# Kernel optimization log

Measured on AMD Instinct MI355X. Metric: run time of the kernel, lower is better.

The kernel has to match this reference:

```python
import jax, jax.numpy as jnp
import numpy as np

B, T, C = 4, 2048, 2048
N_HEAD, N_KV = 16, 4
HEAD_DIM = C // N_HEAD          # 128
KV_DIM = HEAD_DIM * N_KV        # 512
WINDOW = 256
ROPE_BASE = 10000.0


def setup_inputs() -> dict:
    key = jax.random.key(0)
    ks = jax.random.split(key, 5)
    s = 0.02
    return {
        "x": jax.random.normal(ks[0], (B, T, C), dtype=jnp.float32),
        "Wq": jax.random.normal(ks[1], (C, C), dtype=jnp.float32) * s,
        "Wk": jax.random.normal(ks[2], (C, KV_DIM), dtype=jnp.float32) * s,
        "Wv": jax.random.normal(ks[3], (C, KV_DIM), dtype=jnp.float32) * s,
        "Wo": jax.random.normal(ks[4], (C, C), dtype=jnp.float32) * s,
    }


def _rope(x):
    # x: [B, H, T, D]; GPT-NeoX half-split rotation
    d = x.shape[-1]
    t = x.shape[-2]
    inv_freq = 1.0 / (ROPE_BASE ** (jnp.arange(0, d, 2, dtype=jnp.float32) / d))
    freqs = jnp.arange(t, dtype=jnp.float32)[:, None] * inv_freq[None, :]  # [T, D/2]
    cos, sin = jnp.cos(freqs), jnp.sin(freqs)
    x1, x2 = x[..., : d // 2], x[..., d // 2:]
    return jnp.concatenate([x1 * cos - x2 * sin, x1 * sin + x2 * cos], axis=-1)


def reference(x, Wq, Wk, Wv, Wo):
    b, t, c = x.shape
    hd = HEAD_DIM
    q = (x @ Wq).reshape(b, t, N_HEAD, hd).transpose(0, 2, 1, 3)   # [B,nh,T,hd]
    k = (x @ Wk).reshape(b, t, N_KV, hd).transpose(0, 2, 1, 3)     # [B,nkv,T,hd]
    v = (x @ Wv).reshape(b, t, N_KV, hd).transpose(0, 2, 1, 3)

    q = _rope(q)
    k = _rope(k)

    # GQA: repeat kv heads to match query heads
    rep = N_HEAD // N_KV
    k = jnp.repeat(k, rep, axis=1)   # [B,nh,T,hd]
    v = jnp.repeat(v, rep, axis=1)

    att = jnp.einsum("bhqd,bhkd->bhqk", q, k) / jnp.sqrt(jnp.float32(hd))
    i = jnp.arange(t)[:, None]
    j = jnp.arange(t)[None, :]
    # causal AND sliding window: i - WINDOW <= j <= i
    mask = (j <= i) & (j >= i - WINDOW)
    att = jnp.where(mask[None, None], att, jnp.finfo(att.dtype).min)
    att = jax.nn.softmax(att, axis=-1)

    y = jnp.einsum("bhqk,bhkd->bhqd", att, v)          # [B,nh,T,hd]
    y = y.transpose(0, 2, 1, 3).reshape(b, t, c)       # [B,T,C]
    return y @ Wo
```

## Files before the change

### kernel.cpp

```cpp
#include <hip/hip_runtime.h>
#include <stdint.h>

#define T_ 2048
#define C_ 2048
#define HD 128
#define LDQKV 3072

typedef unsigned short u16;
typedef __attribute__((ext_vector_type(8))) short bf16x8;
typedef __attribute__((ext_vector_type(4))) float f32x4;
typedef __attribute__((ext_vector_type(4))) float float4v;
typedef __attribute__((ext_vector_type(4))) u16 u16x4;
typedef __attribute__((ext_vector_type(8))) u16 u16x8;

typedef __attribute__((address_space(3))) void lds_void;
typedef const __attribute__((address_space(1))) void gbl_void;

__device__ __forceinline__ void gload_lds16(const void* g, void* l) {
  __builtin_amdgcn_global_load_lds((gbl_void*)(uintptr_t)g,
                                   (lds_void*)(uint32_t)(uintptr_t)l, 16, 0, 0);
}

__device__ __forceinline__ u16 f2bf(float f) {
  union { float f; uint32_t u; } v; v.f = f;
  uint32_t r = v.u + 0x7FFFu + ((v.u >> 16) & 1u);
  return (u16)(r >> 16);
}
__device__ __forceinline__ float bf2f(u16 h) {
  union { uint32_t u; float f; } v; v.u = ((uint32_t)h) << 16;
  return v.f;
}

#define BAR() do { asm volatile("" ::: "memory"); __builtin_amdgcn_s_barrier(); asm volatile("" ::: "memory"); } while (0)
#define VMCNT(n) asm volatile("s_waitcnt vmcnt(" #n ")" ::: "memory")
#define LGKM0()  asm volatile("s_waitcnt lgkmcnt(0)" ::: "memory")

__global__ __launch_bounds__(256) void k_conv_x(const float* __restrict__ x, u16* __restrict__ o) {
  size_t idx = (size_t)blockIdx.x * 256 + threadIdx.x;
  float4v xv = *(const float4v*)(x + idx * 4);
  u16x4 r;
#pragma unroll
  for (int e = 0; e < 4; ++e) r[e] = f2bf(xv[e]);
  *(u16x4*)(o + idx * 4) = r;
}

__device__ __forceinline__ void ttile(const float* __restrict__ src, int ldw, int nb,
                                      int k0, int n0out, u16* __restrict__ out, int tid,
                                      float (*Lt)[68]) {
  int kr = tid >> 4, nc = (tid & 15) * 4;
#pragma unroll
  for (int s = 0; s < 4; ++s) {
    float4v v = *(const float4v*)(src + (size_t)(k0 + kr + 16 * s) * ldw + nb + nc);
#pragma unroll
    for (int e = 0; e < 4; ++e) Lt[kr + 16 * s][nc + e] = v[e];
  }
  __syncthreads();
  int nr = tid & 31, kc = (tid >> 5) * 8;
#pragma unroll
  for (int s2 = 0; s2 < 2; ++s2) {
    int n = nr + 32 * s2;
    u16x8 o;
#pragma unroll
    for (int e = 0; e < 8; ++e) o[e] = f2bf(Lt[kc + e][n]);
    *(u16x8*)(out + (size_t)(n0out + n) * 2048 + k0 + kc) = o;
  }
}

__global__ __launch_bounds__(256) void k_wt_qkv(const float* __restrict__ Wq, const float* __restrict__ Wk,
                                                const float* __restrict__ Wv, u16* __restrict__ wt) {
  __shared__ float Lt[64][68];
  const int n0 = blockIdx.x * 64, k0 = blockIdx.y * 64;
  const float* src; int ldw, nb;
  if (n0 < 2048)      { src = Wq; ldw = 2048; nb = n0; }
  else if (n0 < 2560) { src = Wk; ldw = 512;  nb = n0 - 2048; }
  else                { src = Wv; ldw = 512;  nb = n0 - 2560; }
  ttile(src, ldw, nb, k0, n0, wt, threadIdx.x, Lt);
}

__global__ __launch_bounds__(256) void k_wo_t(const float* __restrict__ Wo, u16* __restrict__ wt) {
  __shared__ float Lt[64][68];
  ttile(Wo, 2048, blockIdx.x * 64, blockIdx.y * 64, blockIdx.x * 64, wt, threadIdx.x, Lt);
}

__global__ __launch_bounds__(256) void k_cs(float* __restrict__ cst) {
  int idx = blockIdx.x * 256 + threadIdx.x;
  int t = idx >> 6, d = idx & 63;
  float inv = expf(-(float)d * (1.0f / 64.0f) * 9.2103403719761836f);
  float f = (float)t * inv;
  float s, c;
  sincosf(f, &s, &c);
  cst[idx * 2] = c;
  cst[idx * 2 + 1] = s;
}

__global__ __launch_bounds__(256) void k_rope(u16* __restrict__ qkv, const float* __restrict__ cst) {
  int idx = blockIdx.x * 256 + threadIdx.x;
  int token = idx / 160;
  int rem = idx - token * 160;
  int hd = rem >> 3, oct = rem & 7;
  int col = ((hd < 16) ? hd * 128 : 2048 + (hd - 16) * 128) + oct * 8;
  size_t base = (size_t)token * LDQKV + col;
  int t = token & (T_ - 1);
  float sc = (hd < 16) ? 0.08838834764831845f : 1.0f;
  u16x8 a = *(const u16x8*)(qkv + base);
  u16x8 b2 = *(const u16x8*)(qkv + base + 64);
  const float* cp = cst + (size_t)(t * 64 + oct * 8) * 2;
  u16x8 ra, rb;
#pragma unroll
  for (int e = 0; e < 8; ++e) {
    float c = cp[e * 2], s = cp[e * 2 + 1];
    float x1 = bf2f(a[e]), x2 = bf2f(b2[e]);
    ra[e] = f2bf((x1 * c - x2 * s) * sc);
    rb[e] = f2bf((x1 * s + x2 * c) * sc);
  }
  *(u16x8*)(qkv + base) = ra;
  *(u16x8*)(qkv + base + 64) = rb;
}

#define READ_A(mf, ks) (*(const bf16x8*)&As_[(wm * 128 + (mf) * 16 + l15) * 64 + ((((ks) * 4 + lhi) ^ (l15 & 7)) * 8)])
#define READ_B(nf, ks) (*(const bf16x8*)&Bs_[(wn * 64 + (nf) * 16 + l15) * 64 + ((((ks) * 4 + lhi) ^ (l15 & 7)) * 8)])
#define MFMA_QUAD(Q)                                                          \
  _Pragma("unroll") for (int mi = 0; mi < 2; ++mi)                            \
  _Pragma("unroll") for (int nf = 0; nf < 4; ++nf)                            \
  _Pragma("unroll") for (int ks = 0; ks < 2; ++ks)                            \
      acc[(Q) * 2 + mi][nf] = __builtin_amdgcn_mfma_f32_16x16x32_bf16(        \
          af[(Q) * 2 + mi][ks], bb[nf][ks], acc[(Q) * 2 + mi][nf], 0, 0, 0);

template<int OUTF32>
__global__ __launch_bounds__(512, 2) void k_gemm8(const u16* __restrict__ A, const u16* __restrict__ Bt,
                                                  void* __restrict__ Cout, int M, int N, int K, int nbx) {
  __shared__ __attribute__((aligned(16))) u16 lds[2][2][256 * 64];
  const int tid = threadIdx.x, lane = tid & 63;
  const int w = tid >> 6, wm = w >> 2, wn = w & 3;
  const int l15 = lane & 15, lhi = lane >> 4;
  const int nwg = gridDim.x, cpx = nwg >> 3;
  const int wg = (blockIdx.x & 7) * cpx + (blockIdx.x >> 3);
  const int bx = wg % nbx, by = wg / nbx;
  const int m0 = by * 256, n0 = bx * 256;
  const int NT = K >> 6;

  auto STAGE = [&](int half, int tt) {
    const u16* src = (half < 2) ? A : Bt;
    const int r0 = ((half < 2) ? m0 : n0) + (half & 1) * 128;
    u16* dst = &lds[tt & 1][half >> 1][(half & 1) * 8192];
    const int kk = tt * 64;
#pragma unroll
    for (int it = 0; it < 2; ++it) {
      int c = it * 512 + tid;
      int row = c >> 3, kc = c & 7;
      gload_lds16(src + (size_t)(r0 + row) * K + kk + ((kc ^ (row & 7)) * 8), dst + c * 8);
    }
  };

  f32x4 acc[8][4];
#pragma unroll
  for (int i = 0; i < 8; ++i)
#pragma unroll
    for (int j = 0; j < 4; ++j) acc[i][j] = (f32x4){0.f, 0.f, 0.f, 0.f};

  STAGE(0, 0); STAGE(1, 0); STAGE(2, 0); STAGE(3, 0);
  STAGE(0, 1); STAGE(1, 1); STAGE(2, 1);
  VMCNT(6);
  BAR();

  for (int t = 0; t < NT; ++t) {
    const u16* As_ = lds[t & 1][0];
    const u16* Bs_ = lds[t & 1][1];
    bf16x8 af[8][2], bb[4][2];
#pragma unroll
    for (int nf = 0; nf < 4; ++nf) { bb[nf][0] = READ_B(nf, 0); bb[nf][1] = READ_B(nf, 1); }
#pragma unroll
    for (int mf = 0; mf < 2; ++mf) { af[mf][0] = READ_A(mf, 0); af[mf][1] = READ_A(mf, 1); }
    if (t + 1 < NT) STAGE(3, t + 1);
    BAR();
    __builtin_amdgcn_s_setprio(1);
    MFMA_QUAD(0);
    __builtin_amdgcn_s_setprio(0);
    BAR();
#pragma unroll
    for (int mf = 2; mf < 8; ++mf) { af[mf][0] = READ_A(mf, 0); af[mf][1] = READ_A(mf, 1); }
    if (t + 2 < NT) STAGE(2, t + 2);
    BAR();
    __builtin_amdgcn_s_setprio(1);
    MFMA_QUAD(1);
    __builtin_amdgcn_s_setprio(0);
    LGKM0();
    BAR();
    if (t + 2 < NT) STAGE(0, t + 2);
    BAR();
    __builtin_amdgcn_s_setprio(1);
    MFMA_QUAD(2);
    __builtin_amdgcn_s_setprio(0);
    BAR();
    if (t + 2 < NT) STAGE(1, t + 2);
    BAR();
    __builtin_amdgcn_s_setprio(1);
    MFMA_QUAD(3);
    __builtin_amdgcn_s_setprio(0);
    if (t + 2 < NT) { VMCNT(6); } else { VMCNT(0); }
    BAR();
  }

#pragma unroll
  for (int mf = 0; mf < 8; ++mf) {
#pragma unroll
    for (int nf = 0; nf < 4; ++nf) {
      int col = n0 + wn * 64 + nf * 16 + l15;
#pragma unroll
      for (int r = 0; r < 4; ++r) {
        int row = m0 + wm * 128 + mf * 16 + lhi * 4 + r;
        float v = acc[mf][nf][r];
        if (OUTF32) ((float*)Cout)[(size_t)row * N + col] = v;
        else        ((u16*)Cout)[(size_t)row * N + col] = f2bf(v);
      }
    }
  }
}

__global__ __launch_bounds__(256) void k_attn(const u16* __restrict__ qkv, u16* __restrict__ y) {
  const int bid = blockIdx.x;
  const int qt = bid & 31, h = (bid >> 5) & 15, b = bid >> 9;
  const int i0 = qt * 64;
  const size_t tb = (size_t)b * T_ * LDQKV;
  const u16* qb = qkv + tb + h * HD;
  const u16* kb = qkv + tb + 2048 + (h >> 2) * HD;
  const u16* vb = kb + 512;
  __shared__ __attribute__((aligned(16))) u16 smem[20480];
  u16* Ks = smem;
  u16* Vt = smem + 8192;
  u16* Psw = smem + 16384;
  u16* Qs = smem;
  const int tid = threadIdx.x, lane = tid & 63, w = tid >> 6;
  const int l15 = lane & 15, lhi = lane >> 4;
  u16* Ps = Psw + w * 1024;

#pragma unroll
  for (int it = 0; it < 4; ++it) {
    int c = it * 256 + tid, row = c >> 4, kc = (c & 15) ^ (row & 7);
    gload_lds16(qb + (size_t)(i0 + row) * LDQKV + kc * 8, &Qs[(it * 256 + w * 64) * 8]);
  }
  __syncthreads();
  bf16x8 qf[4];
#pragma unroll
  for (int ks = 0; ks < 4; ++ks) {
    int row = w * 16 + l15;
    int kc = (ks * 4 + lhi) ^ (row & 7);
    qf[ks] = *(const bf16x8*)&Qs[(row * 16 + kc) * 8];
  }
  __syncthreads();

  f32x4 o[8];
#pragma unroll
  for (int dt = 0; dt < 8; ++dt) o[dt] = (f32x4){0.f, 0.f, 0.f, 0.f};
  float mrun[4], lrun[4];
#pragma unroll
  for (int r = 0; r < 4; ++r) { mrun[r] = -1e30f; lrun[r] = 0.f; }

  const int jb0 = (i0 >= 256) ? (i0 - 256) : 0;
  for (int jb = jb0; jb <= i0; jb += 64) {
#pragma unroll
    for (int it = 0; it < 4; ++it) {
      int c = it * 256 + tid, row = c >> 4, kc = (c & 15) ^ (row & 7);
      gload_lds16(kb + (size_t)(jb + row) * LDQKV + kc * 8, &Ks[(it * 256 + w * 64) * 8]);
    }
#pragma unroll
    for (int it = 0; it < 4; ++it) {
      int chunk = it * 256 + tid, row = chunk >> 4, dc = chunk & 15;
      u16x8 vv = *(const u16x8*)(vb + (size_t)(jb + row) * LDQKV + dc * 8);
#pragma unroll
      for (int e = 0; e < 8; ++e) {
        int d = dc * 8 + e;
        int s = (dc ^ e) & 7;
        Vt[d * 64 + (row ^ (s << 3))] = vv[e];
      }
    }
    __syncthreads();

    f32x4 s[4];
#pragma unroll
    for (int t = 0; t < 4; ++t) {
      s[t] = (f32x4){0.f, 0.f, 0.f, 0.f};
#pragma unroll
      for (int ks = 0; ks < 4; ++ks) {
        int row = t * 16 + l15;
        int kc = (ks * 4 + lhi) ^ (row & 7);
        bf16x8 kf = *(const bf16x8*)&Ks[(row * 16 + kc) * 8];
        s[t] = __builtin_amdgcn_mfma_f32_16x16x32_bf16(qf[ks], kf, s[t], 0, 0, 0);
      }
    }

    const int irow0 = i0 + w * 16 + lhi * 4;
    float rmax[4];
#pragma unroll
    for (int r = 0; r < 4; ++r) rmax[r] = -1e30f;
#pragma unroll
    for (int t = 0; t < 4; ++t) {
      int j = jb + t * 16 + l15;
#pragma unroll
      for (int r = 0; r < 4; ++r) {
        int i = irow0 + r;
        float sv = s[t][r];
        sv = (j <= i && j + 256 >= i) ? sv : -1e30f;
        s[t][r] = sv;
        rmax[r] = fmaxf(rmax[r], sv);
      }
    }
#pragma unroll
    for (int r = 0; r < 4; ++r) {
#pragma unroll
      for (int off = 1; off < 16; off <<= 1)
        rmax[r] = fmaxf(rmax[r], __shfl_xor(rmax[r], off));
    }
    float sf[4], psum[4];
#pragma unroll
    for (int r = 0; r < 4; ++r) {
      float mn = fmaxf(mrun[r], rmax[r]);
      sf[r] = __expf(mrun[r] - mn);
      mrun[r] = mn;
      psum[r] = 0.f;
    }
#pragma unroll
    for (int t = 0; t < 4; ++t) {
#pragma unroll
      for (int r = 0; r < 4; ++r) {
        float p = __expf(s[t][r] - mrun[r]);
        psum[r] += p;
        int q = lhi * 4 + r;
        int k = t * 16 + l15;
        Ps[q * 64 + (k ^ ((q & 7) << 3))] = f2bf(p);
      }
    }
#pragma unroll
    for (int r = 0; r < 4; ++r) {
#pragma unroll
      for (int off = 1; off < 16; off <<= 1)
        psum[r] += __shfl_xor(psum[r], off);
      lrun[r] = lrun[r] * sf[r] + psum[r];
    }
#pragma unroll
    for (int dt = 0; dt < 8; ++dt)
#pragma unroll
      for (int r = 0; r < 4; ++r)
        o[dt][r] = o[dt][r] * sf[r];

    bf16x8 pf[2];
#pragma unroll
    for (int ks2 = 0; ks2 < 2; ++ks2)
      pf[ks2] = *(const bf16x8*)&Ps[l15 * 64 + ((ks2 * 32 + lhi * 8) ^ ((l15 & 7) << 3))];
#pragma unroll
    for (int dt = 0; dt < 8; ++dt) {
#pragma unroll
      for (int ks2 = 0; ks2 < 2; ++ks2) {
        int d = dt * 16 + l15;
        int s2 = ((d >> 3) ^ (d & 7)) & 7;
        bf16x8 vf = *(const bf16x8*)&Vt[d * 64 + ((ks2 * 32 + lhi * 8) ^ (s2 << 3))];
        o[dt] = __builtin_amdgcn_mfma_f32_16x16x32_bf16(pf[ks2], vf, o[dt], 0, 0, 0);
      }
    }
    __syncthreads();
  }

#pragma unroll
  for (int dt = 0; dt < 8; ++dt) {
#pragma unroll
    for (int r = 0; r < 4; ++r) {
      int i = i0 + w * 16 + lhi * 4 + r;
      float v = o[dt][r] / lrun[r];
      y[((size_t)b * T_ + i) * C_ + h * HD + dt * 16 + l15] = f2bf(v);
    }
  }
}

extern "C" void kernel_launch(void* const* d_in, const int* in_sizes, int n_in,
                              void* d_out, int out_size, void* d_ws, size_t ws_size,
                              hipStream_t stream) {
  const float* x  = (const float*)d_in[0];
  const float* Wq = (const float*)d_in[1];
  const float* Wk = (const float*)d_in[2];
  const float* Wv = (const float*)d_in[3];
  const float* Wo = (const float*)d_in[4];
  char* ws = (char*)d_ws;
  u16* x_bf   = (u16*)(ws);
  u16* wt_qkv = (u16*)(ws + 33554432);
  u16* wo_t   = (u16*)(ws + 46137344);
  u16* qkv    = (u16*)(ws + 54525952);
  float* cst  = (float*)(ws + 104857600);
  u16* ybuf = x_bf;

  k_conv_x <<<16384, 256, 0, stream>>>(x, x_bf);
  k_wt_qkv <<<dim3(48, 32), 256, 0, stream>>>(Wq, Wk, Wv, wt_qkv);
  k_wo_t   <<<dim3(32, 32), 256, 0, stream>>>(Wo, wo_t);
  k_cs     <<<512, 256, 0, stream>>>(cst);

  k_gemm8<0><<<384, 512, 0, stream>>>(x_bf, wt_qkv, (void*)qkv, 8192, 3072, 2048, 12);

  k_rope   <<<5120, 256, 0, stream>>>(qkv, cst);
  k_attn   <<<2048, 256, 0, stream>>>(qkv, ybuf);

  k_gemm8<1><<<256, 512, 0, stream>>>(ybuf, wo_t, d_out, 8192, 2048, 2048, 8);
}
```

Baseline: 310.0 us.

## Software-pipeline GEMM LDS reads with ping-pong B fragments across k-tiles

Restructures the GEMM main loop so the next tile's B fragments and first A fragments are read from LDS during the current tile's MFMA quads. Two B register sets alternate and the loop is unrolled by two. This cuts barriers per tile and reorders global-to-LDS staging with new vmcnt thresholds, aiming to hide LDS latency behind MFMA work. It costs more registers (an extra bf16x8[4][2] set) under a 512x2 launch bound, which risks spills. It also assumes NT is even.

```diff
diff --git a/kernel.cpp b/kernel.cpp
--- a/kernel.cpp
+++ b/kernel.cpp
@@ -117,14 +117,12 @@
   *(u16x8*)(qkv + base + 64) = rb;
 }
 
-#define READ_A(mf, ks) (*(const bf16x8*)&As_[(wm * 128 + (mf) * 16 + l15) * 64 + ((((ks) * 4 + lhi) ^ (l15 & 7)) * 8)])
-#define READ_B(nf, ks) (*(const bf16x8*)&Bs_[(wn * 64 + (nf) * 16 + l15) * 64 + ((((ks) * 4 + lhi) ^ (l15 & 7)) * 8)])
-#define MFMA_QUAD(Q)                                                          \
+#define MQ(Q, BB)                                                             \
   _Pragma("unroll") for (int mi = 0; mi < 2; ++mi)                            \
   _Pragma("unroll") for (int nf = 0; nf < 4; ++nf)                            \
   _Pragma("unroll") for (int ks = 0; ks < 2; ++ks)                            \
       acc[(Q) * 2 + mi][nf] = __builtin_amdgcn_mfma_f32_16x16x32_bf16(        \
-          af[(Q) * 2 + mi][ks], bb[nf][ks], acc[(Q) * 2 + mi][nf], 0, 0, 0);
+          af[(Q) * 2 + mi][ks], BB[nf][ks], acc[(Q) * 2 + mi][nf], 0, 0, 0);
 
 template<int OUTF32>
 __global__ __launch_bounds__(512, 2) void k_gemm8(const u16* __restrict__ A, const u16* __restrict__ Bt,
@@ -151,6 +149,12 @@
       gload_lds16(src + (size_t)(r0 + row) * K + kk + ((kc ^ (row & 7)) * 8), dst + c * 8);
     }
   };
+  auto RA = [&](const u16* buf, int mf, int ks) -> bf16x8 {
+    return *(const bf16x8*)&buf[(wm * 128 + mf * 16 + l15) * 64 + (((ks * 4 + lhi) ^ (l15 & 7)) * 8)];
+  };
+  auto RB = [&](const u16* buf, int nf, int ks) -> bf16x8 {
+    return *(const bf16x8*)&buf[(wn * 64 + nf * 16 + l15) * 64 + (((ks * 4 + lhi) ^ (l15 & 7)) * 8)];
+  };
 
   f32x4 acc[8][4];
 #pragma unroll
@@ -158,47 +162,72 @@
 #pragma unroll
     for (int j = 0; j < 4; ++j) acc[i][j] = (f32x4){0.f, 0.f, 0.f, 0.f};
 
+  bf16x8 af[8][2], bbA[4][2], bbB[4][2];
+
   STAGE(0, 0); STAGE(1, 0); STAGE(2, 0); STAGE(3, 0);
-  STAGE(0, 1); STAGE(1, 1); STAGE(2, 1);
-  VMCNT(6);
+  STAGE(2, 1); STAGE(3, 1); STAGE(0, 1); STAGE(1, 1);
+  VMCNT(8);
   BAR();
-
-  for (int t = 0; t < NT; ++t) {
-    const u16* As_ = lds[t & 1][0];
-    const u16* Bs_ = lds[t & 1][1];
-    bf16x8 af[8][2], bb[4][2];
-#pragma unroll
-    for (int nf = 0; nf < 4; ++nf) { bb[nf][0] = READ_B(nf, 0); bb[nf][1] = READ_B(nf, 1); }
-#pragma unroll
-    for (int mf = 0; mf < 2; ++mf) { af[mf][0] = READ_A(mf, 0); af[mf][1] = READ_A(mf, 1); }
-    if (t + 1 < NT) STAGE(3, t + 1);
-    BAR();
+#pragma unroll
+  for (int ks = 0; ks < 2; ++ks) {
+    af[0][ks] = RA(lds[0][0], 0, ks);
+    af[1][ks] = RA(lds[0][0], 1, ks);
+#pragma unroll
+    for (int nf = 0; nf < 4; ++nf) bbA[nf][ks] = RB(lds[0][1], nf, ks);
+  }
+  LGKM0();
+  BAR();
+
+  auto TILE = [&](int t, bf16x8 (&bbc)[4][2], bf16x8 (&bbn)[4][2]) {
+    const u16* Ac = lds[t & 1][0];
+    const u16* An = lds[(t + 1) & 1][0];
+    const u16* Bn = lds[(t + 1) & 1][1];
+    const bool hasN1 = (t + 1 < NT), hasN2 = (t + 2 < NT);
+    if (hasN2) STAGE(2, t + 2);
+#pragma unroll
+    for (int ks = 0; ks < 2; ++ks) { af[2][ks] = RA(Ac, 2, ks); af[3][ks] = RA(Ac, 3, ks); }
     __builtin_amdgcn_s_setprio(1);
-    MFMA_QUAD(0);
+    MQ(0, bbc);
     __builtin_amdgcn_s_setprio(0);
-    BAR();
-#pragma unroll
-    for (int mf = 2; mf < 8; ++mf) { af[mf][0] = READ_A(mf, 0); af[mf][1] = READ_A(mf, 1); }
-    if (t + 2 < NT) STAGE(2, t + 2);
-    BAR();
+    LGKM0(); BAR();
+    if (hasN2) STAGE(3, t + 2);
+#pragma unroll
+    for (int ks = 0; ks < 2; ++ks) { af[4][ks] = RA(Ac, 4, ks); af[5][ks] = RA(Ac, 5, ks); }
     __builtin_amdgcn_s_setprio(1);
-    MFMA_QUAD(1);
+    MQ(1, bbc);
     __builtin_amdgcn_s_setprio(0);
     LGKM0();
+    if (hasN2) { VMCNT(8); } else { VMCNT(0); }
     BAR();
-    if (t + 2 < NT) STAGE(0, t + 2);
+#pragma unroll
+    for (int ks = 0; ks < 2; ++ks) { af[6][ks] = RA(Ac, 6, ks); af[7][ks] = RA(Ac, 7, ks); }
+    if (hasN1) {
+#pragma unroll
+      for (int ks = 0; ks < 2; ++ks) { bbn[0][ks] = RB(Bn, 0, ks); bbn[1][ks] = RB(Bn, 1, ks); }
+    }
+    __builtin_amdgcn_s_setprio(1);
+    MQ(2, bbc);
+    __builtin_amdgcn_s_setprio(0);
+    LGKM0();
+    if (hasN2) { VMCNT(4); } else { VMCNT(0); }
     BAR();
+    if (hasN2) { STAGE(0, t + 2); STAGE(1, t + 2); }
+    if (hasN1) {
+#pragma unroll
+      for (int ks = 0; ks < 2; ++ks) {
+        af[0][ks] = RA(An, 0, ks); af[1][ks] = RA(An, 1, ks);
+        bbn[2][ks] = RB(Bn, 2, ks); bbn[3][ks] = RB(Bn, 3, ks);
+      }
+    }
     __builtin_amdgcn_s_setprio(1);
-    MFMA_QUAD(2);
+    MQ(3, bbc);
     __builtin_amdgcn_s_setprio(0);
-    BAR();
-    if (t + 2 < NT) STAGE(1, t + 2);
-    BAR();
-    __builtin_amdgcn_s_setprio(1);
-    MFMA_QUAD(3);
-    __builtin_amdgcn_s_setprio(0);
-    if (t + 2 < NT) { VMCNT(6); } else { VMCNT(0); }
-    BAR();
+    LGKM0(); BAR();
+  };
+
+  for (int tp = 0; tp < NT; tp += 2) {
+    TILE(tp, bbA, bbB);
+    TILE(tp + 1, bbB, bbA);
   }
 
 #pragma unroll
```

Measured after the change: 722.1 us. +132.9%, slower.

## Restructure GEMM pipeline to read A fragments per quadrant and reorder staging

Applied to the files above, without the earlier changes.

Rewrites the k_gemm8 main loop so A fragments are loaded from LDS two m-fragments at a time right before each MFMA quadrant, instead of holding all eight in registers. The order of global-to-LDS staging changes: the A halves for t+1 and the B halves for t+2 are interleaved between quadrants, and the vmcnt threshold moves to match. Launch bounds drop to one workgroup per CU, which raises the register budget but lowers occupancy. The aim is to reduce register pressure and spread LDS reads across the loop to overlap with compute, at the cost of more barriers and LDS wait points.

```diff
diff --git a/kernel.cpp b/kernel.cpp
--- a/kernel.cpp
+++ b/kernel.cpp
@@ -117,17 +117,15 @@
   *(u16x8*)(qkv + base + 64) = rb;
 }
 
-#define READ_A(mf, ks) (*(const bf16x8*)&As_[(wm * 128 + (mf) * 16 + l15) * 64 + ((((ks) * 4 + lhi) ^ (l15 & 7)) * 8)])
-#define READ_B(nf, ks) (*(const bf16x8*)&Bs_[(wn * 64 + (nf) * 16 + l15) * 64 + ((((ks) * 4 + lhi) ^ (l15 & 7)) * 8)])
-#define MFMA_QUAD(Q)                                                          \
+#define MQ(Q)                                                                 \
   _Pragma("unroll") for (int mi = 0; mi < 2; ++mi)                            \
   _Pragma("unroll") for (int nf = 0; nf < 4; ++nf)                            \
   _Pragma("unroll") for (int ks = 0; ks < 2; ++ks)                            \
       acc[(Q) * 2 + mi][nf] = __builtin_amdgcn_mfma_f32_16x16x32_bf16(        \
-          af[(Q) * 2 + mi][ks], bb[nf][ks], acc[(Q) * 2 + mi][nf], 0, 0, 0);
+          aa[mi][ks], bb[nf][ks], acc[(Q) * 2 + mi][nf], 0, 0, 0);
 
 template<int OUTF32>
-__global__ __launch_bounds__(512, 2) void k_gemm8(const u16* __restrict__ A, const u16* __restrict__ Bt,
+__global__ __launch_bounds__(512, 1) void k_gemm8(const u16* __restrict__ A, const u16* __restrict__ Bt,
                                                   void* __restrict__ Cout, int M, int N, int K, int nbx) {
   __shared__ __attribute__((aligned(16))) u16 lds[2][2][256 * 64];
   const int tid = threadIdx.x, lane = tid & 63;
@@ -151,6 +149,12 @@
       gload_lds16(src + (size_t)(r0 + row) * K + kk + ((kc ^ (row & 7)) * 8), dst + c * 8);
     }
   };
+  auto RA = [&](const u16* buf, int mf, int ks) -> bf16x8 {
+    return *(const bf16x8*)&buf[(wm * 128 + mf * 16 + l15) * 64 + (((ks * 4 + lhi) ^ (l15 & 7)) * 8)];
+  };
+  auto RB = [&](const u16* buf, int nf, int ks) -> bf16x8 {
+    return *(const bf16x8*)&buf[(wn * 64 + nf * 16 + l15) * 64 + (((ks * 4 + lhi) ^ (l15 & 7)) * 8)];
+  };
 
   f32x4 acc[8][4];
 #pragma unroll
@@ -159,45 +163,49 @@
     for (int j = 0; j < 4; ++j) acc[i][j] = (f32x4){0.f, 0.f, 0.f, 0.f};
 
   STAGE(0, 0); STAGE(1, 0); STAGE(2, 0); STAGE(3, 0);
-  STAGE(0, 1); STAGE(1, 1); STAGE(2, 1);
-  VMCNT(6);
+  STAGE(2, 1); STAGE(3, 1);
+  VMCNT(4);
   BAR();
 
   for (int t = 0; t < NT; ++t) {
-    const u16* As_ = lds[t & 1][0];
-    const u16* Bs_ = lds[t & 1][1];
-    bf16x8 af[8][2], bb[4][2];
-#pragma unroll
-    for (int nf = 0; nf < 4; ++nf) { bb[nf][0] = READ_B(nf, 0); bb[nf][1] = READ_B(nf, 1); }
-#pragma unroll
-    for (int mf = 0; mf < 2; ++mf) { af[mf][0] = READ_A(mf, 0); af[mf][1] = READ_A(mf, 1); }
-    if (t + 1 < NT) STAGE(3, t + 1);
-    BAR();
+    const u16* Ab = lds[t & 1][0];
+    const u16* Bb = lds[t & 1][1];
+    const bool hasN1 = (t + 1 < NT), hasN2 = (t + 2 < NT);
+    bf16x8 bb[4][2], aa[2][2];
+#pragma unroll
+    for (int nf = 0; nf < 4; ++nf) { bb[nf][0] = RB(Bb, nf, 0); bb[nf][1] = RB(Bb, nf, 1); }
+#pragma unroll
+    for (int ks = 0; ks < 2; ++ks) { aa[0][ks] = RA(Ab, 0, ks); aa[1][ks] = RA(Ab, 1, ks); }
+    if (hasN1) STAGE(0, t + 1);
+    BAR(); LGKM0();
     __builtin_amdgcn_s_setprio(1);
-    MFMA_QUAD(0);
+    MQ(0);
     __builtin_amdgcn_s_setprio(0);
     BAR();
 #pragma unroll
-    for (int mf = 2; mf < 8; ++mf) { af[mf][0] = READ_A(mf, 0); af[mf][1] = READ_A(mf, 1); }
-    if (t + 2 < NT) STAGE(2, t + 2);
-    BAR();
+    for (int ks = 0; ks < 2; ++ks) { aa[0][ks] = RA(Ab, 2, ks); aa[1][ks] = RA(Ab, 3, ks); }
+    if (hasN1) STAGE(1, t + 1);
+    BAR(); LGKM0();
     __builtin_amdgcn_s_setprio(1);
-    MFMA_QUAD(1);
-    __builtin_amdgcn_s_setprio(0);
-    LGKM0();
-    BAR();
-    if (t + 2 < NT) STAGE(0, t + 2);
-    BAR();
-    __builtin_amdgcn_s_setprio(1);
-    MFMA_QUAD(2);
+    MQ(1);
     __builtin_amdgcn_s_setprio(0);
     BAR();
-    if (t + 2 < NT) STAGE(1, t + 2);
+#pragma unroll
+    for (int ks = 0; ks < 2; ++ks) { aa[0][ks] = RA(Ab, 4, ks); aa[1][ks] = RA(Ab, 5, ks); }
+    if (hasN2) STAGE(2, t + 2);
+    BAR(); LGKM0();
+    __builtin_amdgcn_s_setprio(1);
+    MQ(2);
+    __builtin_amdgcn_s_setprio(0);
     BAR();
+#pragma unroll
+    for (int ks = 0; ks < 2; ++ks) { aa[0][ks] = RA(Ab, 6, ks); aa[1][ks] = RA(Ab, 7, ks); }
+    if (hasN2) STAGE(3, t + 2);
+    BAR(); LGKM0();
     __builtin_amdgcn_s_setprio(1);
-    MFMA_QUAD(3);
+    MQ(3);
     __builtin_amdgcn_s_setprio(0);
-    if (t + 2 < NT) { VMCNT(6); } else { VMCNT(0); }
+    if (hasN2) { VMCNT(4); } else { VMCNT(0); }
     BAR();
   }
 
```

Result: no change. 313.7 us (+1.2%).
